# Kernel tuning notes

Measured on AMD Instinct MI355X. Metric: run time of the kernel, lower is better.

The kernel has to match this reference:

```python
import jax, jax.numpy as jnp
import numpy as np

N = 100000
E = 1600000
F_IN = 128
H1, C1 = 8, 8          # conv1: 8 heads x 8 channels -> 64
H2, C2 = 1, 16         # conv2: 1 head x num_classes
NEG_SLOPE = 0.2


def setup_inputs() -> dict:
    key = jax.random.key(0)
    ks = jax.random.split(key, 10)
    x = jax.random.normal(ks[0], (N, F_IN), dtype=jnp.float32)
    edge_index = jax.random.randint(ks[1], (2, E), 0, N, dtype=jnp.int64)
    s = 0.1
    return {
        "x": x,
        "edge_index": edge_index,
        "W1": jax.random.normal(ks[2], (F_IN, H1 * C1), dtype=jnp.float32) * s,
        "att_src1": jax.random.normal(ks[3], (H1, C1), dtype=jnp.float32) * s,
        "att_dst1": jax.random.normal(ks[4], (H1, C1), dtype=jnp.float32) * s,
        "b1": jnp.zeros((H1 * C1,), dtype=jnp.float32),
        "W2": jax.random.normal(ks[5], (H1 * C1, H2 * C2), dtype=jnp.float32) * s,
        "att_src2": jax.random.normal(ks[6], (H2, C2), dtype=jnp.float32) * s,
        "att_dst2": jax.random.normal(ks[7], (H2, C2), dtype=jnp.float32) * s,
        "b2": jnp.zeros((H2 * C2,), dtype=jnp.float32),
    }


def gat_conv(x, src, dst, W, a_src, a_dst, bias, heads, out_ch):
    n = x.shape[0]
    h = (x @ W).reshape(n, heads, out_ch)            # [N,H,C]
    alpha_s = jnp.einsum("nhc,hc->nh", h, a_src)      # [N,H]
    alpha_d = jnp.einsum("nhc,hc->nh", h, a_dst)
    e = jax.nn.leaky_relu(alpha_s[src] + alpha_d[dst], NEG_SLOPE)  # [Etot,H]
    # segment softmax over edges grouped by destination node
    e_max = jax.ops.segment_max(e, dst, num_segments=n)
    w = jnp.exp(e - e_max[dst])
    denom = jax.ops.segment_sum(w, dst, num_segments=n)
    alpha = w / denom[dst]                            # [Etot,H]
    msg = h[src] * alpha[:, :, None]                  # [Etot,H,C]
    out = jax.ops.segment_sum(msg, dst, num_segments=n)
    return out.reshape(n, heads * out_ch) + bias


def reference(x, edge_index, W1, att_src1, att_dst1, b1, W2, att_src2, att_dst2, b2):
    # PyG GATConv adds self-loops by default
    loops = jnp.arange(N, dtype=edge_index.dtype)
    src = jnp.concatenate([edge_index[0], loops])
    dst = jnp.concatenate([edge_index[1], loops])
    # dropout layers are identity in eval mode
    h = gat_conv(x, src, dst, W1, att_src1, att_dst1, b1, H1, C1)
    h = jax.nn.elu(h)
    out = gat_conv(h, src, dst, W2, att_src2, att_dst2, b2, H2, C2)
    return out
```

## Files before the change

### kernel.cpp

```cpp
#include <hip/hip_runtime.h>

#define NEG_SLOPE 0.2f
#define BKT 64
#define SHIFT 9
#define CAP 10240

typedef __attribute__((ext_vector_type(8))) short bf16x8;
typedef __attribute__((ext_vector_type(4))) float f32x4;

__device__ __forceinline__ unsigned short f2bf(float f) {
    unsigned u = __float_as_uint(f);
    return (unsigned short)((u + 0x7FFFu + ((u >> 16) & 1u)) >> 16);
}
__device__ __forceinline__ float bf2f(unsigned short h) {
    return __uint_as_float((unsigned)h << 16);
}
__device__ __forceinline__ unsigned pack_bf16(float a, float b) {
    unsigned ua = __float_as_uint(a), ub = __float_as_uint(b);
    ua = (ua + 0x7FFFu + ((ua >> 16) & 1u)) >> 16;
    ub = (ub + 0x7FFFu + ((ub >> 16) & 1u)) & 0xFFFF0000u;
    return ua | ub;
}
__device__ __forceinline__ float bflo(unsigned v) { return __uint_as_float(v << 16); }
__device__ __forceinline__ float bfhi(unsigned v) { return __uint_as_float(v & 0xFFFF0000u); }

__global__ void wext_kernel(const float* __restrict__ W1, const float* __restrict__ as_,
                            const float* __restrict__ ad_, unsigned short* __restrict__ wext) {
    int i = blockIdx.x * 256 + threadIdx.x;
    if (i >= 128 * 80) return;
    int k = i / 80, c = i % 80;
    float v;
    if (c < 64) {
        v = W1[k * 64 + c];
    } else if (c < 72) {
        int h = c - 64; v = 0.f;
        for (int q = 0; q < 8; ++q) v += W1[k * 64 + h * 8 + q] * as_[h * 8 + q];
    } else {
        int h = c - 72; v = 0.f;
        for (int q = 0; q < 8; ++q) v += W1[k * 64 + h * 8 + q] * ad_[h * 8 + q];
    }
    wext[i] = f2bf(v);
}

__global__ __launch_bounds__(256) void fat_kernel(
    const float* __restrict__ x, const unsigned short* __restrict__ wext,
    unsigned* __restrict__ h1bf, float* __restrict__ as1, float* __restrict__ ad1,
    const int* __restrict__ src, const int* __restrict__ dst,
    int* __restrict__ cursor, int* __restrict__ bucket,
    int* __restrict__ gcur, int2* __restrict__ binned,
    int n, int ntiles, int gemm_blocks, int E, int Etot, int nbins, int mode) {
    if ((int)blockIdx.x < gemm_blocks) {
        int lane = threadIdx.x & 63;
        int r = lane & 15, g = lane >> 4;
        bf16x8 wf[4][5];
#pragma unroll
        for (int ks = 0; ks < 4; ++ks)
#pragma unroll
            for (int nt = 0; nt < 5; ++nt) {
                const unsigned short* wp = wext + (size_t)(ks * 32 + g * 8) * 80 + nt * 16 + r;
#pragma unroll
                for (int i = 0; i < 8; ++i) wf[ks][nt][i] = (short)wp[(size_t)i * 80];
            }
        int nwaves = gemm_blocks * 4;
        int w = blockIdx.x * 4 + (threadIdx.x >> 6);
        for (int t = w; t < ntiles; t += nwaves) {
            int row = t * 16 + r;
            int rowc = row < n ? row : n - 1;
            const float* xp = x + (size_t)rowc * 128 + g * 8;
            float4 fa[4], fb[4];
#pragma unroll
            for (int ks = 0; ks < 4; ++ks) {
                fa[ks] = *(const float4*)(xp + ks * 32);
                fb[ks] = *(const float4*)(xp + ks * 32 + 4);
            }
            f32x4 acc[5];
#pragma unroll
            for (int nt = 0; nt < 5; ++nt) acc[nt] = (f32x4){0.f, 0.f, 0.f, 0.f};
#pragma unroll
            for (int ks = 0; ks < 4; ++ks) {
                float f[8];
                f[0] = fa[ks].x; f[1] = fa[ks].y; f[2] = fa[ks].z; f[3] = fa[ks].w;
                f[4] = fb[ks].x; f[5] = fb[ks].y; f[6] = fb[ks].z; f[7] = fb[ks].w;
                bf16x8 ah, al;
#pragma unroll
                for (int i = 0; i < 8; ++i) {
                    unsigned short hb = f2bf(f[i]);
                    ah[i] = (short)hb;
                    al[i] = (short)f2bf(f[i] - bf2f(hb));
                }
#pragma unroll
                for (int nt = 0; nt < 5; ++nt)
                    acc[nt] = __builtin_amdgcn_mfma_f32_16x16x32_bf16(ah, wf[ks][nt], acc[nt], 0, 0, 0);
#pragma unroll
                for (int nt = 0; nt < 5; ++nt)
                    acc[nt] = __builtin_amdgcn_mfma_f32_16x16x32_bf16(al, wf[ks][nt], acc[nt], 0, 0, 0);
            }
#pragma unroll
            for (int reg = 0; reg < 4; ++reg) {
                int nrow = t * 16 + g * 4 + reg;
                bool live = nrow < n;
#pragma unroll
                for (int nt = 0; nt < 4; ++nt) {
                    float v = acc[nt][reg];
                    float o = __shfl_xor(v, 1, 64);
                    if (live && !(r & 1))
                        h1bf[(size_t)nrow * 32 + nt * 8 + (r >> 1)] = pack_bf16(v, o);
                }
                float v4 = acc[4][reg];
                if (live) {
                    if (r < 8) as1[(size_t)nrow * 8 + r] = v4;
                    else       ad1[(size_t)nrow * 8 + (r - 8)] = v4;
                }
            }
        }
    } else if (mode == 2) {
        __shared__ int lhist[256];
        __shared__ int lbase[256];
        int t = threadIdx.x;
        int blk = (int)blockIdx.x - gemm_blocks;
        lhist[t] = 0;
        __syncthreads();
        int e0 = blk * 2048;
        int d[8], s[8], lo[8];
        bool val[8];
#pragma unroll
        for (int j = 0; j < 8; ++j) {
            int e = e0 + j * 256 + t;
            val[j] = e < Etot;
            d[j] = s[j] = 0;
            if (val[j]) {
                if (e < E) { s[j] = src[e]; d[j] = dst[e]; }
                else { s[j] = d[j] = e - E; }
                lo[j] = atomicAdd(&lhist[d[j] >> SHIFT], 1);
            }
        }
        __syncthreads();
        if (t < nbins && lhist[t] > 0) lbase[t] = atomicAdd(&gcur[t], lhist[t]);
        __syncthreads();
#pragma unroll
        for (int j = 0; j < 8; ++j) {
            if (val[j]) {
                int bin = d[j] >> SHIFT;
                int pos = lbase[bin] + lo[j];
                if (pos < CAP) binned[(size_t)bin * CAP + pos] = make_int2(d[j], s[j]);
            }
        }
    } else {
        int tid = ((int)blockIdx.x - gemm_blocks) * 256 + threadIdx.x;
        int T = ((int)gridDim.x - gemm_blocks) * 256;
        int s[8], d[8], p[8];
        bool v[8];
#pragma unroll
        for (int j = 0; j < 8; ++j) {
            int e = tid + j * T;
            v[j] = e < Etot;
            s[j] = d[j] = 0;
            if (v[j]) {
                if (e < E) { s[j] = src[e]; d[j] = dst[e]; }
                else { s[j] = d[j] = e - E; }
            }
        }
#pragma unroll
        for (int j = 0; j < 8; ++j)
            if (v[j]) p[j] = atomicAdd(&cursor[d[j]], 1);
#pragma unroll
        for (int j = 0; j < 8; ++j)
            if (v[j] && p[j] < BKT) bucket[(size_t)d[j] * BKT + p[j]] = s[j];
    }
}

__global__ __launch_bounds__(512) void binB_kernel(const int* __restrict__ gcur,
                                                   const int2* __restrict__ binned,
                                                   int* __restrict__ bucket,
                                                   int* __restrict__ cursor, int n) {
    __shared__ int lcur[512];
    int bin = blockIdx.x;
    int t = threadIdx.x;
    lcur[t] = 0;
    __syncthreads();
    int cnt = gcur[bin];
    if (cnt > CAP) cnt = CAP;
    const int2* bp = binned + (size_t)bin * CAP;
    for (int k = t; k < cnt; k += 512) {
        int2 p = bp[k];
        int slot = atomicAdd(&lcur[p.x & 511], 1);
        if (slot < BKT) bucket[(size_t)p.x * BKT + slot] = p.y;
    }
    __syncthreads();
    int node = (bin << SHIFT) + t;
    if (node < n) cursor[node] = min(lcur[t], BKT);
}

__global__ void agg1_kernel(const int* __restrict__ cursor, const int* __restrict__ edges,
                            const float* __restrict__ as1, const float* __restrict__ ad1,
                            const uint4* __restrict__ h1bf4, const float* __restrict__ b1,
                            const float* __restrict__ W2, const float* __restrict__ as2w,
                            const float* __restrict__ ad2w, unsigned* __restrict__ h2bf,
                            float* __restrict__ as2, float* __restrict__ ad2, int n) {
    __shared__ float sW[64 * 17];
    for (int i = threadIdx.x; i < 64 * 16; i += blockDim.x)
        sW[(i >> 4) * 17 + (i & 15)] = W2[i];
    __syncthreads();
    int gtid = blockIdx.x * blockDim.x + threadIdx.x;
    int node = gtid >> 6;
    int lane = threadIdx.x & 63;
    if (node >= n) return;
    int g8 = lane >> 3, u = lane & 7;
    int cnt = min(cursor[node], BKT);
    const int* ed = edges + (size_t)node * BKT;
    int ed_reg = ed[lane];
    float adv = ad1[(size_t)node * 8 + u];
    float a0 = 0.f, a1 = 0.f, a2 = 0.f, a3 = 0.f;
    float a4 = 0.f, a5 = 0.f, a6 = 0.f, a7 = 0.f, wsum = 0.f;
#pragma unroll
    for (int i = 0; i < 8; ++i) {
        int k = i * 8 + g8;
        int s = __shfl(ed_reg, k, 64);
        if (k < cnt) {
            float a = as1[(size_t)s * 8 + u] + adv;
            float ee = a > 0.f ? a : NEG_SLOPE * a;
            float w = __expf(ee);
            uint4 v = h1bf4[(size_t)s * 8 + u];
            a0 += w * bflo(v.x); a1 += w * bfhi(v.x);
            a2 += w * bflo(v.y); a3 += w * bfhi(v.y);
            a4 += w * bflo(v.z); a5 += w * bfhi(v.z);
            a6 += w * bflo(v.w); a7 += w * bfhi(v.w);
            wsum += w;
        }
    }
#pragma unroll
    for (int off = 8; off <= 32; off <<= 1) {
        a0 += __shfl_xor(a0, off, 64); a1 += __shfl_xor(a1, off, 64);
        a2 += __shfl_xor(a2, off, 64); a3 += __shfl_xor(a3, off, 64);
        a4 += __shfl_xor(a4, off, 64); a5 += __shfl_xor(a5, off, 64);
        a6 += __shfl_xor(a6, off, 64); a7 += __shfl_xor(a7, off, 64);
        wsum += __shfl_xor(wsum, off, 64);
    }
    float inv = 1.f / wsum;
    float4 bb0 = ((const float4*)b1)[2 * u];
    float4 bb1 = ((const float4*)b1)[2 * u + 1];
    float e0 = a0 * inv + bb0.x, e1 = a1 * inv + bb0.y;
    float e2 = a2 * inv + bb0.z, e3 = a3 * inv + bb0.w;
    float e4 = a4 * inv + bb1.x, e5 = a5 * inv + bb1.y;
    float e6 = a6 * inv + bb1.z, e7 = a7 * inv + bb1.w;
    e0 = e0 > 0.f ? e0 : __expf(e0) - 1.f;
    e1 = e1 > 0.f ? e1 : __expf(e1) - 1.f;
    e2 = e2 > 0.f ? e2 : __expf(e2) - 1.f;
    e3 = e3 > 0.f ? e3 : __expf(e3) - 1.f;
    e4 = e4 > 0.f ? e4 : __expf(e4) - 1.f;
    e5 = e5 > 0.f ? e5 : __expf(e5) - 1.f;
    e6 = e6 > 0.f ? e6 : __expf(e6) - 1.f;
    e7 = e7 > 0.f ? e7 : __expf(e7) - 1.f;
    int gg = lane >> 4, c = lane & 15;
    float hv = 0.f;
    float q0, q1;
    q0 = __shfl(e0, 2 * gg, 64); q1 = __shfl(e0, 2 * gg + 1, 64);
    hv += q0 * sW[(16 * gg + 0) * 17 + c] + q1 * sW[(16 * gg + 8) * 17 + c];
    q0 = __shfl(e1, 2 * gg, 64); q1 = __shfl(e1, 2 * gg + 1, 64);
    hv += q0 * sW[(16 * gg + 1) * 17 + c] + q1 * sW[(16 * gg + 9) * 17 + c];
    q0 = __shfl(e2, 2 * gg, 64); q1 = __shfl(e2, 2 * gg + 1, 64);
    hv += q0 * sW[(16 * gg + 2) * 17 + c] + q1 * sW[(16 * gg + 10) * 17 + c];
    q0 = __shfl(e3, 2 * gg, 64); q1 = __shfl(e3, 2 * gg + 1, 64);
    hv += q0 * sW[(16 * gg + 3) * 17 + c] + q1 * sW[(16 * gg + 11) * 17 + c];
    q0 = __shfl(e4, 2 * gg, 64); q1 = __shfl(e4, 2 * gg + 1, 64);
    hv += q0 * sW[(16 * gg + 4) * 17 + c] + q1 * sW[(16 * gg + 12) * 17 + c];
    q0 = __shfl(e5, 2 * gg, 64); q1 = __shfl(e5, 2 * gg + 1, 64);
    hv += q0 * sW[(16 * gg + 5) * 17 + c] + q1 * sW[(16 * gg + 13) * 17 + c];
    q0 = __shfl(e6, 2 * gg, 64); q1 = __shfl(e6, 2 * gg + 1, 64);
    hv += q0 * sW[(16 * gg + 6) * 17 + c] + q1 * sW[(16 * gg + 14) * 17 + c];
    q0 = __shfl(e7, 2 * gg, 64); q1 = __shfl(e7, 2 * gg + 1, 64);
    hv += q0 * sW[(16 * gg + 7) * 17 + c] + q1 * sW[(16 * gg + 15) * 17 + c];
    hv += __shfl_xor(hv, 16, 64);
    hv += __shfl_xor(hv, 32, 64);
    float v0 = __shfl(hv, 2 * (lane & 7), 64);
    float v1 = __shfl(hv, 2 * (lane & 7) + 1, 64);
    if (lane < 8) h2bf[(size_t)node * 8 + lane] = pack_bf16(v0, v1);
    float ts = hv * as2w[c], td = hv * ad2w[c];
    ts += __shfl_xor(ts, 1, 64); td += __shfl_xor(td, 1, 64);
    ts += __shfl_xor(ts, 2, 64); td += __shfl_xor(td, 2, 64);
    ts += __shfl_xor(ts, 4, 64); td += __shfl_xor(td, 4, 64);
    ts += __shfl_xor(ts, 8, 64); td += __shfl_xor(td, 8, 64);
    if (lane == 0) { as2[node] = ts; ad2[node] = td; }
}

__global__ void agg2_kernel(const int* __restrict__ cursor, const int* __restrict__ edges,
                            const float* __restrict__ as2, const float* __restrict__ ad2,
                            const uint2* __restrict__ h2bf2, const float* __restrict__ b2,
                            float* __restrict__ out, int n) {
    int gtid = blockIdx.x * blockDim.x + threadIdx.x;
    int node = gtid >> 6;
    int lane = threadIdx.x & 63;
    if (node >= n) return;
    int g = lane >> 2, u = lane & 3;
    int cnt = min(cursor[node], BKT);
    const int* ed = edges + (size_t)node * BKT;
    int ed_reg = ed[lane];
    float adv = ad2[node];
    float a0 = 0.f, a1 = 0.f, a2 = 0.f, a3 = 0.f, wsum = 0.f;
#pragma unroll
    for (int i = 0; i < 4; ++i) {
        int k = i * 16 + g;
        int s = __shfl(ed_reg, k, 64);
        if (k < cnt) {
            float a = as2[s] + adv;
            float ee = a > 0.f ? a : NEG_SLOPE * a;
            float w = __expf(ee);
            uint2 v = h2bf2[(size_t)s * 4 + u];
            a0 += w * bflo(v.x);
            a1 += w * bfhi(v.x);
            a2 += w * bflo(v.y);
            a3 += w * bfhi(v.y);
            wsum += w;
        }
    }
#pragma unroll
    for (int off = 4; off <= 32; off <<= 1) {
        a0 += __shfl_xor(a0, off, 64); a1 += __shfl_xor(a1, off, 64);
        a2 += __shfl_xor(a2, off, 64); a3 += __shfl_xor(a3, off, 64);
        wsum += __shfl_xor(wsum, off, 64);
    }
    if (lane < 4) {
        float inv = 1.f / wsum;
        float4 bb = ((const float4*)b2)[u];
        ((float4*)out)[(size_t)node * 4 + u] =
            make_float4(a0 * inv + bb.x, a1 * inv + bb.y, a2 * inv + bb.z, a3 * inv + bb.w);
    }
}

extern "C" void kernel_launch(void* const* d_in, const int* in_sizes, int n_in,
                              void* d_out, int out_size, void* d_ws, size_t ws_size,
                              hipStream_t stream) {
    const float* x      = (const float*)d_in[0];
    const int*   ei     = (const int*)d_in[1];
    const float* W1     = (const float*)d_in[2];
    const float* att_s1 = (const float*)d_in[3];
    const float* att_d1 = (const float*)d_in[4];
    const float* b1     = (const float*)d_in[5];
    const float* W2     = (const float*)d_in[6];
    const float* att_s2 = (const float*)d_in[7];
    const float* att_d2 = (const float*)d_in[8];
    const float* b2     = (const float*)d_in[9];

    int N_   = in_sizes[0] / 128;
    int E_   = in_sizes[1] / 2;
    int Etot = E_ + N_;
    const int* srcA = ei;
    const int* dstA = ei + E_;

    unsigned short* wext = (unsigned short*)d_ws;
    unsigned* h1bf = (unsigned*)(wext + 128 * 80);
    float* as1   = (float*)(h1bf + (size_t)N_ * 32);
    float* ad1   = as1 + (size_t)N_ * 8;
    unsigned* h2bf = (unsigned*)(ad1 + (size_t)N_ * 8);
    float* as2   = (float*)(h2bf + (size_t)N_ * 8);
    float* ad2   = as2 + (size_t)N_;
    int*   cursor = (int*)(ad2 + (size_t)N_);
    int*   bucket = cursor + N_;
    int*   gcur   = bucket + (size_t)N_ * BKT;
    int2*  binned = (int2*)(gcur + 256);

    int nbins = (N_ + (1 << SHIFT) - 1) >> SHIFT;
    size_t need_bucket = 20480 + (size_t)N_ * (32 + 8 + 8 + 8 + 1 + 1 + 1 + BKT) * 4;
    size_t need_binned = need_bucket + 1024 + (size_t)nbins * CAP * 8;
    bool use_bucket = ws_size >= need_bucket;
    bool use_binned = (ws_size >= need_binned) && (nbins <= 256);

    int ntiles = (N_ + 15) / 16;
    int GB1 = (ntiles + 15) / 16;
    int GB2 = (Etot + 2047) / 2048;
    int nb_wave = ((size_t)N_ * 64 + 255) / 256;

    wext_kernel<<<40, 256, 0, stream>>>(W1, att_s1, att_d1, wext);

    if (use_binned) {
        hipMemsetAsync(gcur, 0, (size_t)nbins * sizeof(int), stream);
        fat_kernel<<<GB1 + GB2, 256, 0, stream>>>(x, wext, h1bf, as1, ad1, srcA, dstA,
                                                  cursor, bucket, gcur, binned,
                                                  N_, ntiles, GB1, E_, Etot, nbins, 2);
        binB_kernel<<<nbins, 512, 0, stream>>>(gcur, binned, bucket, cursor, N_);
    } else if (use_bucket) {
        hipMemsetAsync(cursor, 0, (size_t)N_ * sizeof(int), stream);
        fat_kernel<<<GB1 + GB2, 256, 0, stream>>>(x, wext, h1bf, as1, ad1, srcA, dstA,
                                                  cursor, bucket, nullptr, nullptr,
                                                  N_, ntiles, GB1, E_, Etot, nbins, 1);
    } else {
        return;
    }

    agg1_kernel<<<nb_wave, 256, 0, stream>>>(cursor, bucket, as1, ad1,
                                             (const uint4*)h1bf, b1, W2, att_s2, att_d2,
                                             h2bf, as2, ad2, N_);
    agg2_kernel<<<nb_wave, 256, 0, stream>>>(cursor, bucket, as2, ad2,
                                             (const uint2*)h2bf, b2, (float*)d_out, N_);
}
```

Baseline: 170.5 us.

## Process two nodes per wave in agg1 with dynamic edge-count loop

```diff
diff --git a/kernel.cpp b/kernel.cpp
--- a/kernel.cpp
+++ b/kernel.cpp
@@ -201,22 +201,26 @@
     for (int i = threadIdx.x; i < 64 * 16; i += blockDim.x)
         sW[(i >> 4) * 17 + (i & 15)] = W2[i];
     __syncthreads();
-    int gtid = blockIdx.x * blockDim.x + threadIdx.x;
-    int node = gtid >> 6;
+    int wave = (blockIdx.x * blockDim.x + threadIdx.x) >> 6;
+    int pair = wave * 2;
+    if (pair >= n) return;
     int lane = threadIdx.x & 63;
-    if (node >= n) return;
-    int g8 = lane >> 3, u = lane & 7;
-    int cnt = min(cursor[node], BKT);
-    const int* ed = edges + (size_t)node * BKT;
-    int ed_reg = ed[lane];
-    float adv = ad1[(size_t)node * 8 + u];
+    int hbase = lane & 32;
+    int l5 = lane & 31, g = l5 >> 3, u = l5 & 7;
+    int node = pair + (lane >> 5);
+    bool valid = node < n;
+    int nodec = valid ? node : pair;
+    int cnt = valid ? min(cursor[nodec], BKT) : 0;
+    const int* ed = edges + (size_t)nodec * BKT;
+    int edlo = ed[l5];
+    int edhi = ed[32 + l5];
+    float adv = ad1[(size_t)nodec * 8 + u];
+    int cntmax = max(cnt, __shfl_xor(cnt, 32, 64));
     float a0 = 0.f, a1 = 0.f, a2 = 0.f, a3 = 0.f;
     float a4 = 0.f, a5 = 0.f, a6 = 0.f, a7 = 0.f, wsum = 0.f;
-#pragma unroll
-    for (int i = 0; i < 8; ++i) {
-        int k = i * 8 + g8;
-        int s = __shfl(ed_reg, k, 64);
-        if (k < cnt) {
+    for (int k0 = 0; k0 < cntmax; k0 += 4) {
+        int s = __shfl(k0 < 32 ? edlo : edhi, hbase + ((k0 + g) & 31), 64);
+        if (k0 + g < cnt) {
             float a = as1[(size_t)s * 8 + u] + adv;
             float ee = a > 0.f ? a : NEG_SLOPE * a;
             float w = __expf(ee);
@@ -229,7 +233,7 @@
         }
     }
 #pragma unroll
-    for (int off = 8; off <= 32; off <<= 1) {
+    for (int off = 8; off <= 16; off <<= 1) {
         a0 += __shfl_xor(a0, off, 64); a1 += __shfl_xor(a1, off, 64);
         a2 += __shfl_xor(a2, off, 64); a3 += __shfl_xor(a3, off, 64);
         a4 += __shfl_xor(a4, off, 64); a5 += __shfl_xor(a5, off, 64);
@@ -251,36 +255,32 @@
     e5 = e5 > 0.f ? e5 : __expf(e5) - 1.f;
     e6 = e6 > 0.f ? e6 : __expf(e6) - 1.f;
     e7 = e7 > 0.f ? e7 : __expf(e7) - 1.f;
-    int gg = lane >> 4, c = lane & 15;
+    int gg = l5 >> 4, c = l5 & 15;
     float hv = 0.f;
-    float q0, q1;
-    q0 = __shfl(e0, 2 * gg, 64); q1 = __shfl(e0, 2 * gg + 1, 64);
-    hv += q0 * sW[(16 * gg + 0) * 17 + c] + q1 * sW[(16 * gg + 8) * 17 + c];
-    q0 = __shfl(e1, 2 * gg, 64); q1 = __shfl(e1, 2 * gg + 1, 64);
-    hv += q0 * sW[(16 * gg + 1) * 17 + c] + q1 * sW[(16 * gg + 9) * 17 + c];
-    q0 = __shfl(e2, 2 * gg, 64); q1 = __shfl(e2, 2 * gg + 1, 64);
-    hv += q0 * sW[(16 * gg + 2) * 17 + c] + q1 * sW[(16 * gg + 10) * 17 + c];
-    q0 = __shfl(e3, 2 * gg, 64); q1 = __shfl(e3, 2 * gg + 1, 64);
-    hv += q0 * sW[(16 * gg + 3) * 17 + c] + q1 * sW[(16 * gg + 11) * 17 + c];
-    q0 = __shfl(e4, 2 * gg, 64); q1 = __shfl(e4, 2 * gg + 1, 64);
-    hv += q0 * sW[(16 * gg + 4) * 17 + c] + q1 * sW[(16 * gg + 12) * 17 + c];
-    q0 = __shfl(e5, 2 * gg, 64); q1 = __shfl(e5, 2 * gg + 1, 64);
-    hv += q0 * sW[(16 * gg + 5) * 17 + c] + q1 * sW[(16 * gg + 13) * 17 + c];
-    q0 = __shfl(e6, 2 * gg, 64); q1 = __shfl(e6, 2 * gg + 1, 64);
-    hv += q0 * sW[(16 * gg + 6) * 17 + c] + q1 * sW[(16 * gg + 14) * 17 + c];
-    q0 = __shfl(e7, 2 * gg, 64); q1 = __shfl(e7, 2 * gg + 1, 64);
-    hv += q0 * sW[(16 * gg + 7) * 17 + c] + q1 * sW[(16 * gg + 15) * 17 + c];
+#pragma unroll
+    for (int m = 0; m < 4; ++m) {
+        int usrc = hbase + 4 * gg + m;
+        int rbase = (4 * gg + m) * 8;
+        float q;
+        q = __shfl(e0, usrc, 64); hv += q * sW[(rbase + 0) * 17 + c];
+        q = __shfl(e1, usrc, 64); hv += q * sW[(rbase + 1) * 17 + c];
+        q = __shfl(e2, usrc, 64); hv += q * sW[(rbase + 2) * 17 + c];
+        q = __shfl(e3, usrc, 64); hv += q * sW[(rbase + 3) * 17 + c];
+        q = __shfl(e4, usrc, 64); hv += q * sW[(rbase + 4) * 17 + c];
+        q = __shfl(e5, usrc, 64); hv += q * sW[(rbase + 5) * 17 + c];
+        q = __shfl(e6, usrc, 64); hv += q * sW[(rbase + 6) * 17 + c];
+        q = __shfl(e7, usrc, 64); hv += q * sW[(rbase + 7) * 17 + c];
+    }
     hv += __shfl_xor(hv, 16, 64);
-    hv += __shfl_xor(hv, 32, 64);
-    float v0 = __shfl(hv, 2 * (lane & 7), 64);
-    float v1 = __shfl(hv, 2 * (lane & 7) + 1, 64);
-    if (lane < 8) h2bf[(size_t)node * 8 + lane] = pack_bf16(v0, v1);
+    float v0 = __shfl(hv, hbase + 2 * u, 64);
+    float v1 = __shfl(hv, hbase + 2 * u + 1, 64);
+    if (valid && l5 < 8) h2bf[(size_t)node * 8 + l5] = pack_bf16(v0, v1);
     float ts = hv * as2w[c], td = hv * ad2w[c];
     ts += __shfl_xor(ts, 1, 64); td += __shfl_xor(td, 1, 64);
     ts += __shfl_xor(ts, 2, 64); td += __shfl_xor(td, 2, 64);
     ts += __shfl_xor(ts, 4, 64); td += __shfl_xor(td, 4, 64);
     ts += __shfl_xor(ts, 8, 64); td += __shfl_xor(td, 8, 64);
-    if (lane == 0) { as2[node] = ts; ad2[node] = td; }
+    if (valid && l5 == 0) { as2[node] = ts; ad2[node] = td; }
 }
 
 __global__ void agg2_kernel(const int* __restrict__ cursor, const int* __restrict__ edges,
@@ -368,7 +368,8 @@
     int ntiles = (N_ + 15) / 16;
     int GB1 = (ntiles + 15) / 16;
     int GB2 = (Etot + 2047) / 2048;
-    int nb_wave = ((size_t)N_ * 64 + 255) / 256;
+    int nb_wave  = ((size_t)N_ * 64 + 255) / 256;
+    int nb_pair  = (N_ + 7) / 8;
 
     wext_kernel<<<40, 256, 0, stream>>>(W1, att_s1, att_d1, wext);
 
@@ -387,7 +388,7 @@
         return;
     }
 
-    agg1_kernel<<<nb_wave, 256, 0, stream>>>(cursor, bucket, as1, ad1,
+    agg1_kernel<<<nb_pair, 256, 0, stream>>>(cursor, bucket, as1, ad1,
                                              (const uint4*)h1bf, b1, W2, att_s2, att_d2,
                                              h2bf, as2, ad2, N_);
     agg2_kernel<<<nb_wave, 256, 0, stream>>>(cursor, bucket, as2, ad2,
```

New measurement: 152.7 us. -10.4%, faster.
